# Kernel tuning notes

Measured on AMD Instinct MI355X. Metric: run time of the kernel, lower is better.

Reference implementation:

```python
import jax, jax.numpy as jnp
import numpy as np

B = 16384      # rays
H = 128        # field hidden dim


def setup_inputs() -> dict:
    key = jax.random.key(0)
    ks = jax.random.split(key, 8)
    origins = jax.random.normal(ks[0], (B, 3), dtype=jnp.float32)
    directions = jax.random.normal(ks[1], (B, 3), dtype=jnp.float32)
    directions = directions / jnp.linalg.norm(directions, axis=-1, keepdims=True)
    # Field: simple MLP 3 -> H -> H -> 4 (rgb + sigma)
    W1 = jax.random.normal(ks[2], (3, H), dtype=jnp.float32) * (1.0 / np.sqrt(3.0))
    b1 = jnp.zeros((H,), dtype=jnp.float32)
    W2 = jax.random.normal(ks[3], (H, H), dtype=jnp.float32) * (1.0 / np.sqrt(H))
    b2 = jnp.zeros((H,), dtype=jnp.float32)
    W3 = jax.random.normal(ks[4], (H, 4), dtype=jnp.float32) * (1.0 / np.sqrt(H))
    b3 = jnp.zeros((4,), dtype=jnp.float32)
    return {"origins": origins, "directions": directions,
            "W1": W1, "b1": b1, "W2": W2, "b2": b2, "W3": W3, "b3": b3,
            "near": 2, "far": 6, "num_samples": 64}


def _field(x, W1, b1, W2, b2, W3, b3):
    h = jax.nn.relu(x @ W1 + b1)
    h = jax.nn.relu(h @ W2 + b2)
    return h @ W3 + b3


def reference(origins, directions, W1, b1, W2, b2, W3, b3, near, far, num_samples):
    near = jnp.float32(near)
    far = jnp.float32(far)
    # 1. generate_samples: segment boundaries + midpoints along each ray
    depths = jnp.linspace(near, far, num_samples + 1)            # [S+1]
    midpoints = 0.5 * (depths[:-1] + depths[1:])                 # [S]
    # [B, S, 3] = origin + t * direction
    locs = origins[:, None, :] + midpoints[None, :, None] * directions[:, None, :]
    # 2. evaluate field
    f = _field(locs.reshape(-1, 3), W1, b1, W2, b2, W3, b3)
    f = f.reshape(origins.shape[0], num_samples, 4)
    # NOTE: source overwrites the sigmoid'd colors with raw outputs (faithful)
    colors = f[..., :3]                                          # [B, S, 3]
    sigma = f[..., 3]                                            # [B, S]
    # 3. alpha values
    delta = depths[1:] - depths[:-1]                             # [S]
    alphas = 1.0 - jnp.exp(-sigma * delta[None, :])              # [B, S]
    # 4. alpha compositing (black background)
    ones = jnp.ones_like(alphas[:, :1])
    transmittance = jnp.cumprod(jnp.concatenate([ones, 1.0 - alphas], axis=1), axis=1)[:, :-1]
    weights = alphas * transmittance                             # [B, S]
    radiance = jnp.sum(weights[..., None] * colors, axis=1)      # [B, 3]
    return radiance
```

## Files before the change

kernel.cpp:

```cpp
#include <hip/hip_runtime.h>


typedef _Float16 f16;
typedef __attribute__((ext_vector_type(2))) _Float16 h2v;
typedef __attribute__((ext_vector_type(8))) _Float16 half8;
typedef __attribute__((ext_vector_type(4))) float floatx4;

#define H 128
#define NS 64
#define A_STRIDE 132

static __device__ __forceinline__ h2v pkrtz(float a, float b) {
  return __builtin_bit_cast(h2v, __builtin_amdgcn_cvt_pkrtz(a, b));
}

__global__ void nerf_setup(const float* __restrict__ W2, const float* __restrict__ W3,
                           const float* __restrict__ b2,
                           f16* __restrict__ wsW2, f16* __restrict__ wsW3,
                           f16* __restrict__ wsB2) {
  int t = blockIdx.x * blockDim.x + threadIdx.x;
  if (t < 8192) {
    int j2 = t & 3, lane = (t >> 2) & 63, mt = (t >> 8) & 7, ks = t >> 11;
    int k = ks * 32 + ((lane >> 4) * 8) + 2 * j2;
    int n = mt * 16 + (lane & 15);
    wsW2[2 * t]     = (f16)W2[k * H + n];
    wsW2[2 * t + 1] = (f16)W2[(k + 1) * H + n];
  } else if (t < 9216) {
    int u = t - 8192;
    int j2 = u & 3, lane = (u >> 2) & 63, ks = u >> 8;
    int k = ks * 32 + ((lane >> 4) * 8) + 2 * j2;
    int c = lane & 15;
    wsW3[2 * u]     = (c < 4) ? (f16)W3[k * 4 + c]       : (f16)0.0f;
    wsW3[2 * u + 1] = (c < 4) ? (f16)W3[(k + 1) * 4 + c] : (f16)0.0f;
  } else if (t < 9344) {
    int i = t - 9216;
    int b32i = i >> 1, e = i & 1;
    int quad = b32i >> 4, rem = b32i & 15, mt = rem >> 1, p = rem & 1;
    wsB2[i] = (f16)b2[mt * 16 + quad * 4 + 2 * p + e];
  }
}

__global__ __launch_bounds__(256, 3) void nerf_main(
    const float* __restrict__ origins, const float* __restrict__ dirs,
    const float* __restrict__ W1, const float* __restrict__ b1,
    const float* __restrict__ b3,
    const f16* __restrict__ wsW2, const f16* __restrict__ wsW3,
    const f16* __restrict__ wsB2,
    float* __restrict__ out)
{
  __shared__ __align__(16) f16   a_lds[128][A_STRIDE];
  __shared__ __align__(16) f16   popd[4][2][H];
  __shared__ __align__(16) float f_lds[128][4];

  const int t = threadIdx.x;
  const int w = t >> 6, lane = t & 63, quad = lane >> 4, l16 = lane & 15;
  const int prow0 = w * 32;
  const float delta = 4.0f / NS;

  {
    const int ray = blockIdx.x * 2 + (w >> 1);
    const float o0 = origins[ray*3], o1 = origins[ray*3+1], o2 = origins[ray*3+2];
    const float d0 = dirs[ray*3],    d1 = dirs[ray*3+1],    d2 = dirs[ray*3+2];
    const int k0 = lane * 2;
    const float2 wr0 = *(const float2*)&W1[0*H + k0];
    const float2 wr1 = *(const float2*)&W1[1*H + k0];
    const float2 wr2 = *(const float2*)&W1[2*H + k0];
    const float2 bb  = *(const float2*)&b1[k0];
    float poa = fmaf(o2, wr2.x, fmaf(o1, wr1.x, fmaf(o0, wr0.x, bb.x)));
    float pob = fmaf(o2, wr2.y, fmaf(o1, wr1.y, fmaf(o0, wr0.y, bb.y)));
    float pda = fmaf(d2, wr2.x, fmaf(d1, wr1.x, d0 * wr0.x));
    float pdb = fmaf(d2, wr2.y, fmaf(d1, wr1.y, d0 * wr0.y));
    h2v po2; po2[0] = (f16)poa; po2[1] = (f16)pob;
    h2v pd2; pd2[0] = (f16)pda; pd2[1] = (f16)pdb;
    *(h2v*)&popd[w][0][k0] = po2;
    *(h2v*)&popd[w][1][k0] = pd2;
  }

  half8 m8[2];
  #pragma unroll
  for (int tr = 0; tr < 2; ++tr) {
    const int s = (w & 1) * 32 + tr * 16 + l16;
    const f16 m = (f16)(2.0f + (s + 0.5f) * delta);
    m8[tr] = (half8)m;
  }

  floatx4 acc[8][2];
  #pragma unroll
  for (int mt = 0; mt < 8; ++mt) { acc[mt][0] = (floatx4)(0.0f); acc[mt][1] = (floatx4)(0.0f); }

  const half8* w2f = (const half8*)wsW2;
  const half8 z8 = (half8)(f16)0.0f;
  #pragma unroll
  for (int ks = 0; ks < 4; ++ks) {
    half8 aw[8];
    #pragma unroll
    for (int mt = 0; mt < 8; ++mt) aw[mt] = w2f[(ks*8 + mt)*64 + lane];
    const half8 po8 = *(const half8*)&popd[w][0][ks*32 + quad*8];
    const half8 pd8 = *(const half8*)&popd[w][1][ks*32 + quad*8];
    #pragma unroll
    for (int tr = 0; tr < 2; ++tr) {
      half8 hb = pd8 * m8[tr] + po8;
      hb = __builtin_elementwise_max(hb, z8);
      #pragma unroll
      for (int mt = 0; mt < 8; ++mt)
        acc[mt][tr] = __builtin_amdgcn_mfma_f32_16x16x32_f16(aw[mt], hb, acc[mt][tr], 0, 0, 0);
    }
  }

  h2v bpk[8][2];
  {
    const uint2* bp = (const uint2*)wsB2;
    #pragma unroll
    for (int mt = 0; mt < 8; ++mt) {
      union { uint2 u; h2v h[2]; } pk;
      pk.u = bp[quad * 8 + mt];
      bpk[mt][0] = pk.h[0]; bpk[mt][1] = pk.h[1];
    }
  }
  const h2v z2 = (h2v)(f16)0.0f;
  #pragma unroll
  for (int mt = 0; mt < 8; ++mt)
    #pragma unroll
    for (int tr = 0; tr < 2; ++tr) {
      h2v c0 = pkrtz(acc[mt][tr][0], acc[mt][tr][1]);
      h2v c1 = pkrtz(acc[mt][tr][2], acc[mt][tr][3]);
      c0 = __builtin_elementwise_max((h2v)(c0 + bpk[mt][0]), z2);
      c1 = __builtin_elementwise_max((h2v)(c1 + bpk[mt][1]), z2);
      union { h2v h[2]; uint2 u; } pk; pk.h[0] = c0; pk.h[1] = c1;
      *(uint2*)&a_lds[prow0 + tr*16 + l16][mt*16 + quad*4] = pk.u;
    }

  floatx4 acc3[2];
  acc3[0] = (floatx4)(0.0f); acc3[1] = (floatx4)(0.0f);
  const half8* w3f = (const half8*)wsW3;
  half8 w3[4];
  #pragma unroll
  for (int ks = 0; ks < 4; ++ks) w3[ks] = w3f[ks*64 + lane];
  #pragma unroll
  for (int tr = 0; tr < 2; ++tr)
    #pragma unroll
    for (int ks = 0; ks < 4; ++ks) {
      const half8 a = *(const half8*)&a_lds[prow0 + tr*16 + l16][ks*32 + quad*8];
      acc3[tr] = __builtin_amdgcn_mfma_f32_16x16x32_f16(a, w3[ks], acc3[tr], 0, 0, 0);
    }
  if (l16 < 4) {
    const float bc = b3[l16];
    #pragma unroll
    for (int tr = 0; tr < 2; ++tr)
      #pragma unroll
      for (int r = 0; r < 4; ++r)
        f_lds[prow0 + tr*16 + quad*4 + r][l16] = acc3[tr][r] + bc;
  }
  __syncthreads();

  if (w < 2) {
    const int ray = blockIdx.x * 2 + w;
    const float4 fv = *(const float4*)&f_lds[w*64 + lane][0];
    const float sigma = fv.w;
    const float alpha = 1.0f - __expf(-sigma * delta);
    float S = sigma;
    #pragma unroll
    for (int off = 1; off < 64; off <<= 1) {
      float u = __shfl_up(S, off);
      if (lane >= off) S += u;
    }
    const float T  = __expf(-delta * (S - sigma));
    const float wt = alpha * T;
    float cr = wt * fv.x, cg = wt * fv.y, cb = wt * fv.z;
    #pragma unroll
    for (int off = 32; off > 0; off >>= 1) {
      cr += __shfl_down(cr, off);
      cg += __shfl_down(cg, off);
      cb += __shfl_down(cb, off);
    }
    if (lane == 0) {
      out[ray*3+0] = cr; out[ray*3+1] = cg; out[ray*3+2] = cb;
    }
  }
}

extern "C" void kernel_launch(void* const* d_in, const int* in_sizes, int n_in,
                              void* d_out, int out_size, void* d_ws, size_t ws_size,
                              hipStream_t stream) {
  const float* origins = (const float*)d_in[0];
  const float* dirs    = (const float*)d_in[1];
  const float* W1      = (const float*)d_in[2];
  const float* b1      = (const float*)d_in[3];
  const float* W2      = (const float*)d_in[4];
  const float* b2      = (const float*)d_in[5];
  const float* W3      = (const float*)d_in[6];
  const float* b3      = (const float*)d_in[7];
  float* out = (float*)d_out;

  f16* wsW2 = (f16*)d_ws;
  f16* wsW3 = wsW2 + 16384;
  f16* wsB2 = wsW3 + 2048;

  nerf_setup<<<37, 256, 0, stream>>>(W2, W3, b2, wsW2, wsW3, wsB2);
  nerf_main<<<16384 / 2, 256, 0, stream>>>(
      origins, dirs, W1, b1, b3, wsW2, wsW3, wsB2, out);
}
```

Baseline: 119.8 us.

## Give each wavefront a full ray and double-buffer W2 fragment loads

Each wavefront now handles one complete ray of 64 samples instead of half a ray. Every W2 fragment load therefore feeds twice as many MFMAs, and the block-wide barrier is dropped because compositing stays within the wave. W2 fragments for the next k-slice are prefetched into a second register buffer, and the LDS row stride is padded to 136. The cost is doubled accumulator registers (launch bounds lowered to 2 blocks per SIMD) and doubled LDS per block, which lowers occupancy.

```diff
diff --git a/kernel.cpp b/kernel.cpp
--- a/kernel.cpp
+++ b/kernel.cpp
@@ -8,7 +8,7 @@
 
 #define H 128
 #define NS 64
-#define A_STRIDE 132
+#define A_STRIDE 136
 
 static __device__ __forceinline__ h2v pkrtz(float a, float b) {
   return __builtin_bit_cast(h2v, __builtin_amdgcn_cvt_pkrtz(a, b));
@@ -40,7 +40,7 @@
   }
 }
 
-__global__ __launch_bounds__(256, 3) void nerf_main(
+__global__ __launch_bounds__(256, 2) void nerf_main(
     const float* __restrict__ origins, const float* __restrict__ dirs,
     const float* __restrict__ W1, const float* __restrict__ b1,
     const float* __restrict__ b3,
@@ -48,17 +48,17 @@
     const f16* __restrict__ wsB2,
     float* __restrict__ out)
 {
-  __shared__ __align__(16) f16   a_lds[128][A_STRIDE];
+  __shared__ __align__(16) f16   a_lds[256][A_STRIDE];
   __shared__ __align__(16) f16   popd[4][2][H];
-  __shared__ __align__(16) float f_lds[128][4];
+  __shared__ __align__(16) float f_lds[4][64][4];
 
   const int t = threadIdx.x;
   const int w = t >> 6, lane = t & 63, quad = lane >> 4, l16 = lane & 15;
-  const int prow0 = w * 32;
+  const int prow0 = w * 64;
   const float delta = 4.0f / NS;
+  const int ray = blockIdx.x * 4 + w;
 
   {
-    const int ray = blockIdx.x * 2 + (w >> 1);
     const float o0 = origins[ray*3], o1 = origins[ray*3+1], o2 = origins[ray*3+2];
     const float d0 = dirs[ray*3],    d1 = dirs[ray*3+1],    d2 = dirs[ray*3+2];
     const int k0 = lane * 2;
@@ -76,34 +76,40 @@
     *(h2v*)&popd[w][1][k0] = pd2;
   }
 
-  half8 m8[2];
-  #pragma unroll
-  for (int tr = 0; tr < 2; ++tr) {
-    const int s = (w & 1) * 32 + tr * 16 + l16;
-    const f16 m = (f16)(2.0f + (s + 0.5f) * delta);
-    m8[tr] = (half8)m;
-  }
-
-  floatx4 acc[8][2];
-  #pragma unroll
-  for (int mt = 0; mt < 8; ++mt) { acc[mt][0] = (floatx4)(0.0f); acc[mt][1] = (floatx4)(0.0f); }
+  half8 m8[4];
+  #pragma unroll
+  for (int tr = 0; tr < 4; ++tr)
+    m8[tr] = (half8)(f16)(2.0f + (tr*16 + l16 + 0.5f) * delta);
+
+  floatx4 acc[8][4];
+  #pragma unroll
+  for (int mt = 0; mt < 8; ++mt)
+    #pragma unroll
+    for (int tr = 0; tr < 4; ++tr) acc[mt][tr] = (floatx4)(0.0f);
 
   const half8* w2f = (const half8*)wsW2;
   const half8 z8 = (half8)(f16)0.0f;
+  half8 awA[8], awB[8];
+  #pragma unroll
+  for (int mt = 0; mt < 8; ++mt) awA[mt] = w2f[mt*64 + lane];
+
   #pragma unroll
   for (int ks = 0; ks < 4; ++ks) {
-    half8 aw[8];
-    #pragma unroll
-    for (int mt = 0; mt < 8; ++mt) aw[mt] = w2f[(ks*8 + mt)*64 + lane];
+    half8* cur = (ks & 1) ? awB : awA;
+    half8* nxt = (ks & 1) ? awA : awB;
+    if (ks < 3) {
+      #pragma unroll
+      for (int mt = 0; mt < 8; ++mt) nxt[mt] = w2f[((ks+1)*8 + mt)*64 + lane];
+    }
     const half8 po8 = *(const half8*)&popd[w][0][ks*32 + quad*8];
     const half8 pd8 = *(const half8*)&popd[w][1][ks*32 + quad*8];
     #pragma unroll
-    for (int tr = 0; tr < 2; ++tr) {
+    for (int tr = 0; tr < 4; ++tr) {
       half8 hb = pd8 * m8[tr] + po8;
       hb = __builtin_elementwise_max(hb, z8);
       #pragma unroll
       for (int mt = 0; mt < 8; ++mt)
-        acc[mt][tr] = __builtin_amdgcn_mfma_f32_16x16x32_f16(aw[mt], hb, acc[mt][tr], 0, 0, 0);
+        acc[mt][tr] = __builtin_amdgcn_mfma_f32_16x16x32_f16(cur[mt], hb, acc[mt][tr], 0, 0, 0);
     }
   }
 
@@ -121,7 +127,7 @@
   #pragma unroll
   for (int mt = 0; mt < 8; ++mt)
     #pragma unroll
-    for (int tr = 0; tr < 2; ++tr) {
+    for (int tr = 0; tr < 4; ++tr) {
       h2v c0 = pkrtz(acc[mt][tr][0], acc[mt][tr][1]);
       h2v c1 = pkrtz(acc[mt][tr][2], acc[mt][tr][3]);
       c0 = __builtin_elementwise_max((h2v)(c0 + bpk[mt][0]), z2);
@@ -130,14 +136,15 @@
       *(uint2*)&a_lds[prow0 + tr*16 + l16][mt*16 + quad*4] = pk.u;
     }
 
-  floatx4 acc3[2];
-  acc3[0] = (floatx4)(0.0f); acc3[1] = (floatx4)(0.0f);
+  floatx4 acc3[4];
+  #pragma unroll
+  for (int tr = 0; tr < 4; ++tr) acc3[tr] = (floatx4)(0.0f);
   const half8* w3f = (const half8*)wsW3;
   half8 w3[4];
   #pragma unroll
   for (int ks = 0; ks < 4; ++ks) w3[ks] = w3f[ks*64 + lane];
   #pragma unroll
-  for (int tr = 0; tr < 2; ++tr)
+  for (int tr = 0; tr < 4; ++tr)
     #pragma unroll
     for (int ks = 0; ks < 4; ++ks) {
       const half8 a = *(const half8*)&a_lds[prow0 + tr*16 + l16][ks*32 + quad*8];
@@ -146,16 +153,14 @@
   if (l16 < 4) {
     const float bc = b3[l16];
     #pragma unroll
-    for (int tr = 0; tr < 2; ++tr)
+    for (int tr = 0; tr < 4; ++tr)
       #pragma unroll
       for (int r = 0; r < 4; ++r)
-        f_lds[prow0 + tr*16 + quad*4 + r][l16] = acc3[tr][r] + bc;
-  }
-  __syncthreads();
-
-  if (w < 2) {
-    const int ray = blockIdx.x * 2 + w;
-    const float4 fv = *(const float4*)&f_lds[w*64 + lane][0];
+        f_lds[w][tr*16 + quad*4 + r][l16] = acc3[tr][r] + bc;
+  }
+
+  {
+    const float4 fv = *(const float4*)&f_lds[w][lane][0];
     const float sigma = fv.w;
     const float alpha = 1.0f - __expf(-sigma * delta);
     float S = sigma;
@@ -197,6 +202,6 @@
   f16* wsB2 = wsW3 + 2048;
 
   nerf_setup<<<37, 256, 0, stream>>>(W2, W3, b2, wsW2, wsW3, wsB2);
-  nerf_main<<<16384 / 2, 256, 0, stream>>>(
+  nerf_main<<<16384 / 4, 256, 0, stream>>>(
       origins, dirs, W1, b1, b3, wsW2, wsW3, wsB2, out);
 }
```

Result: faster. 111.7 us (-6.7%).
